# Kernel optimization log

Hardware: AMD Instinct MI355X
Metric: run time of the kernel (lower is better)

Reference implementation:

```python
import jax, jax.numpy as jnp
import numpy as np

N = 50000      # nodes
E = 800000     # edges
IN = 32        # raw node feature dim
PE = 15        # laplacian PE dim (k)
HID = 128      # hidden
HEADS = 4
C = HID // HEADS
G = 64         # graphs in batch
L = 4          # num layers (shared weights!)


def setup_inputs() -> dict:
    key = jax.random.key(0)
    ks = jax.random.split(key, 24)
    s = 0.05
    p = lambda k, shape: jax.random.normal(k, shape, dtype=jnp.float32) * s
    inp = {
        "x": jax.random.normal(ks[0], (N, IN), dtype=jnp.float32),
        "edge_index": jax.random.randint(ks[1], (2, E), 0, N, dtype=jnp.int32),
        "batch": jnp.sort(jax.random.randint(ks[2], (N,), 0, G, dtype=jnp.int32)),
        "lap_pe": jax.random.normal(ks[3], (N, PE), dtype=jnp.float32),
        # node_in: Linear(IN+PE -> HID)
        "node_in_w": p(ks[4], (HID, IN + PE)), "node_in_b": p(ks[5], (HID,)),
        # shared TransformerConv params
        "Wq": p(ks[6], (HID, HID)), "bq": p(ks[7], (HID,)),
        "Wk": p(ks[8], (HID, HID)), "bk": p(ks[9], (HID,)),
        "Wv": p(ks[10], (HID, HID)), "bv": p(ks[11], (HID,)),
        "Wskip": p(ks[12], (HID, HID)), "bskip": p(ks[13], (HID,)),
        "Wbeta": p(ks[14], (1, 3 * HID)),  # bias=False in PyG
        # attentional aggregation gate: Linear(HID,HID)->ReLU->Linear(HID,1)
        "g1_w": p(ks[15], (HID, HID)), "g1_b": p(ks[16], (HID,)),
        "g2_w": p(ks[17], (1, HID)), "g2_b": p(ks[18], (1,)),
        # readout: Linear(HID,HID)->ReLU->Linear(HID,1)
        "r1_w": p(ks[19], (HID, HID)), "r1_b": p(ks[20], (HID,)),
        "r2_w": p(ks[21], (1, HID)), "r2_b": p(ks[22], (1,)),
    }
    return inp


def _transformer_conv(x, src, dst, Wq, bq, Wk, bk, Wv, bv, Wskip, bskip, Wbeta):
    # projections -> [N, HEADS, C]
    q = (x @ Wq.T + bq).reshape(N, HEADS, C)
    k = (x @ Wk.T + bk).reshape(N, HEADS, C)
    v = (x @ Wv.T + bv).reshape(N, HEADS, C)
    # edge attention logits: [E, HEADS]
    alpha = jnp.einsum('ehc,ehc->eh', q[dst], k[src]) / jnp.sqrt(jnp.float32(C))
    # segment softmax over destination node
    amax = jax.ops.segment_max(alpha, dst, num_segments=N)        # [N, HEADS]
    ex = jnp.exp(alpha - amax[dst])
    denom = jax.ops.segment_sum(ex, dst, num_segments=N)          # [N, HEADS]
    attn = ex / denom[dst]                                        # [E, HEADS]
    # weighted scatter-add of values
    msg = v[src] * attn[:, :, None]                               # [E, HEADS, C]
    out = jax.ops.segment_sum(msg, dst, num_segments=N).reshape(N, HID)
    # beta-gated skip connection (beta=True, root_weight=True)
    x_r = x @ Wskip.T + bskip
    beta = jax.nn.sigmoid(jnp.concatenate([out, x_r, out - x_r], axis=-1) @ Wbeta.T)
    return beta * x_r + (1.0 - beta) * out


def reference(x, edge_index, batch, lap_pe, node_in_w, node_in_b,
              Wq, bq, Wk, bk, Wv, bv, Wskip, bskip, Wbeta,
              g1_w, g1_b, g2_w, g2_b, r1_w, r1_b, r2_w, r2_b):
    src, dst = edge_index[0], edge_index[1]
    h = jnp.concatenate([x, lap_pe], axis=-1) @ node_in_w.T + node_in_b  # [N, HID]
    for _ in range(L):  # same conv instance reused -> shared weights
        h = jax.nn.relu(h + _transformer_conv(h, src, dst, Wq, bq, Wk, bk,
                                              Wv, bv, Wskip, bskip, Wbeta))
    # attentional aggregation over graphs
    gate = jax.nn.relu(h @ g1_w.T + g1_b) @ g2_w.T + g2_b                # [N, 1]
    gmax = jax.ops.segment_max(gate, batch, num_segments=G)
    gex = jnp.exp(gate - gmax[batch])
    gden = jax.ops.segment_sum(gex, batch, num_segments=G)
    w = gex / gden[batch]                                                # [N, 1]
    g = jax.ops.segment_sum(w * h, batch, num_segments=G)                # [G, HID]
    out = jax.nn.relu(g @ r1_w.T + r1_b) @ r2_w.T + r2_b                 # [G, 1]
    return out.squeeze(-1)
```

## Files before the change

### kernel.cpp

```cpp
#include <hip/hip_runtime.h>

#define NN 50000
#define EE 800000
#define INF 32
#define PEF 15
#define HID 128
#define GG 64
#define NLAYERS 4
#define NBLK 196
#define NBUCK 49
#define ECH 4096
#define EBLK 196

typedef __bf16 bf16;
typedef __attribute__((ext_vector_type(8))) bf16 bf16x8;
typedef __attribute__((ext_vector_type(4))) float f32x4;
typedef __attribute__((ext_vector_type(2))) float f32x2;

__device__ __forceinline__ float wave_allsum(float v) {
  #pragma unroll
  for (int off = 1; off < 64; off <<= 1) v += __shfl_xor(v, off);
  return v;
}

__device__ __forceinline__ float bflo(unsigned u) {
  return __builtin_bit_cast(float, u << 16);
}
__device__ __forceinline__ float bfhi(unsigned u) {
  return __builtin_bit_cast(float, u & 0xffff0000u);
}
__device__ __forceinline__ unsigned short f2bf(float v) {
  unsigned b = __builtin_bit_cast(unsigned, v);
  unsigned r = (b + 0x7fffu + ((b >> 16) & 1u)) >> 16;
  return (unsigned short)r;
}
__device__ __forceinline__ unsigned bfpack(float lo, float hi) {
  return (unsigned)f2bf(lo) | ((unsigned)f2bf(hi) << 16);
}
__device__ __forceinline__ unsigned fp8pack4(float a, float b, float c, float d) {
  unsigned lo = (unsigned)__builtin_amdgcn_cvt_pk_fp8_f32(a, b, 0, false) & 0xffffu;
  unsigned hi = (unsigned)__builtin_amdgcn_cvt_pk_fp8_f32(c, d, 0, false) & 0xffffu;
  return lo | (hi << 16);
}

__global__ void pack_weights_kernel(const float* __restrict__ Wq, const float* __restrict__ Wk,
                                    const float* __restrict__ Wv, const float* __restrict__ Ws,
                                    const float* __restrict__ bq, const float* __restrict__ bk,
                                    const float* __restrict__ bv, const float* __restrict__ bs,
                                    unsigned short* __restrict__ Wcatb, float* __restrict__ bcat) {
  int idx = blockIdx.x * blockDim.x + threadIdx.x;
  if (idx >= 512 * 128) return;
  int o = idx >> 7, j = idx & 127;
  const float* W; const float* b; int r;
  if (o < 128) { W = Wq; b = bq; r = o; }
  else if (o < 384) {
    int g = (o - 128) >> 6, c = (o - 128) & 63;
    if (c < 32) { W = Wk; b = bk; r = 32 * g + c; }
    else        { W = Wv; b = bv; r = 32 * g + (c - 32); }
  } else { W = Ws; b = bs; r = o - 384; }
  Wcatb[idx] = f2bf(W[r * 128 + j]);
  if (j == 0) bcat[o] = b[r];
}

__global__ void pack_nwtb_kernel(const float* __restrict__ niw, unsigned short* __restrict__ nwtb) {
  int idx = blockIdx.x * blockDim.x + threadIdx.x;
  if (idx >= 128 * 64) return;
  int n = idx >> 6, j = idx & 63;
  nwtb[idx] = (j < INF + PEF) ? f2bf(niw[n * (INF + PEF) + j]) : (unsigned short)0;
}

__global__ void pack_g1_kernel(const float* __restrict__ g1w, unsigned short* __restrict__ g1wb) {
  int idx = blockIdx.x * blockDim.x + threadIdx.x;
  if (idx >= 128 * 128) return;
  g1wb[idx] = f2bf(g1w[idx]);
}

__global__ __launch_bounds__(256) void xpe_pack_kernel(const float* __restrict__ x,
    const float* __restrict__ pe, unsigned* __restrict__ xpeb4) {
  int n = blockIdx.x * 256 + threadIdx.x;
  if (n >= NN) return;
  unsigned ou[32];
  const float4* xr = (const float4*)(x + (size_t)n * INF);
  #pragma unroll
  for (int i = 0; i < 8; i++) {
    float4 v = xr[i];
    ou[2 * i] = bfpack(v.x, v.y);
    ou[2 * i + 1] = bfpack(v.z, v.w);
  }
  const float* pr = pe + (size_t)n * PEF;
  float p[16];
  #pragma unroll
  for (int i = 0; i < PEF; i++) p[i] = pr[i];
  p[15] = 0.f;
  #pragma unroll
  for (int i = 0; i < 8; i++) ou[16 + i] = bfpack(p[2 * i], p[2 * i + 1]);
  #pragma unroll
  for (int i = 24; i < 32; i++) ou[i] = 0u;
  unsigned* dst = xpeb4 + (size_t)n * 32;
  #pragma unroll
  for (int i = 0; i < 8; i++) ((uint4*)dst)[i] = *(uint4*)&ou[4 * i];
}

__global__ __launch_bounds__(256) void nodein_gemm_kernel(
    const bf16* __restrict__ A, const bf16* __restrict__ B,
    const float* __restrict__ bias, int M,
    float* __restrict__ h, unsigned* __restrict__ hbf4) {
  __shared__ float lds[128 * 64];
  const int t = threadIdx.x;
  const int w = t >> 6, lane = t & 63;
  const int m0 = blockIdx.x * 128;
  const int n0 = blockIdx.y * 64;
  const int lrow = lane & 15, lk = (lane >> 4) * 8;
  int ra = m0 + w * 32 + lrow;      if (ra > M - 1) ra = M - 1;
  int rb = m0 + w * 32 + 16 + lrow; if (rb > M - 1) rb = M - 1;
  const bf16* a0p = A + (size_t)ra * 64 + lk;
  const bf16* a1p = A + (size_t)rb * 64 + lk;
  const bf16* bp  = B + (size_t)(n0 + lrow) * 64 + lk;
  f32x4 acc[2][4] = {};
  #pragma unroll
  for (int ks = 0; ks < 2; ks++) {
    bf16x8 a0 = *(const bf16x8*)(a0p + ks * 32);
    bf16x8 a1 = *(const bf16x8*)(a1p + ks * 32);
    #pragma unroll
    for (int nj = 0; nj < 4; nj++) {
      bf16x8 b = *(const bf16x8*)(bp + (size_t)nj * 1024 + ks * 32);
      acc[0][nj] = __builtin_amdgcn_mfma_f32_16x16x32_bf16(a0, b, acc[0][nj], 0, 0, 0);
      acc[1][nj] = __builtin_amdgcn_mfma_f32_16x16x32_bf16(a1, b, acc[1][nj], 0, 0, 0);
    }
  }
  const int rbase = (lane >> 4) * 4;
  #pragma unroll
  for (int mi = 0; mi < 2; mi++) {
    #pragma unroll
    for (int nj = 0; nj < 4; nj++) {
      #pragma unroll
      for (int r = 0; r < 4; r++) {
        int ml = w * 32 + mi * 16 + rbase + r;
        int col = nj * 16 + lrow;
        lds[ml * 64 + (col ^ ((ml & 7) << 2))] = acc[mi][nj][r] + bias[n0 + col];
      }
    }
  }
  __syncthreads();
  #pragma unroll
  for (int kk = 0; kk < 2; kk++) {
    int u = t + kk * 256;
    int r = u & 127, s = u >> 7;
    int m = m0 + r;
    if (m >= M) continue;
    float ff[16];
    #pragma unroll
    for (int j = 0; j < 4; j++) {
      int c = s * 16 + j * 4;
      *(float4*)(ff + j * 4) = *(const float4*)(lds + r * 64 + (c ^ ((r & 7) << 2)));
    }
    int c0 = n0 + s * 16;
    float4* hp = (float4*)(h + (size_t)m * 128 + c0);
    #pragma unroll
    for (int j = 0; j < 4; j++) hp[j] = *(float4*)(ff + j * 4);
    unsigned o[8];
    #pragma unroll
    for (int i = 0; i < 8; i++) o[i] = bfpack(ff[2 * i], ff[2 * i + 1]);
    uint4* hb = (uint4*)(hbf4 + (size_t)m * 64 + (c0 >> 1));
    hb[0] = *(uint4*)&o[0];
    hb[1] = *(uint4*)&o[4];
  }
}

__global__ __launch_bounds__(256) void bsum_kernel(const int* __restrict__ counts,
                                                   int* __restrict__ bsum) {
  int b = blockIdx.x, t = threadIdx.x;
  int i = b * 256 + t;
  int v = (i < NN) ? counts[i] : 0;
  #pragma unroll
  for (int off = 1; off < 64; off <<= 1) v += __shfl_xor(v, off);
  __shared__ int red[4];
  if ((t & 63) == 0) red[t >> 6] = v;
  __syncthreads();
  if (t == 0) bsum[b] = red[0] + red[1] + red[2] + red[3];
}

__global__ void bscan_kernel(const int* __restrict__ bsum, int* __restrict__ bbase) {
  int lane = threadIdx.x;
  int carry = 0;
  for (int c = 0; c < NBLK; c += 64) {
    int i = c + lane;
    int v = (i < NBLK) ? bsum[i] : 0;
    int x = v;
    #pragma unroll
    for (int off = 1; off < 64; off <<= 1) {
      int u = __shfl_up(x, off);
      if (lane >= off) x += u;
    }
    if (i < NBLK) bbase[i] = carry + x - v;
    carry += __shfl(x, 63);
  }
}

__global__ __launch_bounds__(256) void rowptr_kernel(const int* __restrict__ counts,
    const int* __restrict__ bbase, int* __restrict__ row_ptr) {
  int b = blockIdx.x, t = threadIdx.x;
  int lane = t & 63, wid = t >> 6;
  int i = b * 256 + t;
  int v = (i < NN) ? counts[i] : 0;
  int x = v;
  #pragma unroll
  for (int off = 1; off < 64; off <<= 1) {
    int u = __shfl_up(x, off);
    if (lane >= off) x += u;
  }
  __shared__ int wsum[4];
  if (lane == 63) wsum[wid] = x;
  __syncthreads();
  int offs = bbase[b];
  for (int k = 0; k < wid; k++) offs += wsum[k];
  int incl = offs + x;
  if (i < NN) row_ptr[i + 1] = incl;
  if (b == 0 && t == 0) row_ptr[0] = 0;
}

__global__ __launch_bounds__(256) void binhist_kernel(const int* __restrict__ dst,
    int* __restrict__ blockHist, int* __restrict__ counts) {
  __shared__ int hist[NBUCK];
  int t = threadIdx.x;
  if (t < NBUCK) hist[t] = 0;
  __syncthreads();
  int base = blockIdx.x * ECH;
  int end = base + ECH; if (end > EE) end = EE;
  for (int i = base + t; i < end; i += 256) {
    int d = dst[i];
    atomicAdd(&hist[d >> 10], 1);
    atomicAdd(&counts[d], 1);
  }
  __syncthreads();
  if (t < NBUCK) blockHist[blockIdx.x * NBUCK + t] = hist[t];
}

__global__ void bscan2_kernel(const int* __restrict__ blockHist,
    int* __restrict__ blockBase, int* __restrict__ bucket_base) {
  int t = threadIdx.x;
  int tot = 0;
  if (t < NBUCK)
    for (int b = 0; b < EBLK; b++) tot += blockHist[b * NBUCK + t];
  int x = tot;
  #pragma unroll
  for (int off = 1; off < 64; off <<= 1) {
    int u = __shfl_up(x, off);
    if (t >= off) x += u;
  }
  int excl = x - tot;
  if (t < NBUCK) bucket_base[t] = excl;
  if (t == NBUCK - 1) bucket_base[NBUCK] = excl + tot;
  if (t < NBUCK) {
    int run = excl;
    for (int b = 0; b < EBLK; b++) {
      blockBase[b * NBUCK + t] = run;
      run += blockHist[b * NBUCK + t];
    }
  }
}

__global__ __launch_bounds__(256) void binwrite_kernel(const int* __restrict__ src,
    const int* __restrict__ dst, const int* __restrict__ blockBase,
    unsigned* __restrict__ binned) {
  __shared__ int cur[NBUCK];
  int t = threadIdx.x;
  if (t < NBUCK) cur[t] = blockBase[blockIdx.x * NBUCK + t];
  __syncthreads();
  int base = blockIdx.x * ECH;
  int end = base + ECH; if (end > EE) end = EE;
  for (int i = base + t; i < end; i += 256) {
    int d = dst[i];
    int p = atomicAdd(&cur[d >> 10], 1);
    binned[p] = (unsigned)src[i] | ((unsigned)(d & 1023) << 16);
  }
}

__global__ __launch_bounds__(512) void scatter2_kernel(const unsigned* __restrict__ binned,
    const int* __restrict__ row_ptr, const int* __restrict__ bucket_base,
    unsigned short* __restrict__ srcs16) {
  __shared__ int cur[1024];
  int g = blockIdx.x, t = threadIdx.x;
  int nbase = g << 10;
  for (int j = t; j < 1024; j += 512) {
    int node = nbase + j;
    cur[j] = (node < NN) ? row_ptr[node] : 0;
  }
  __syncthreads();
  int s0 = bucket_base[g], s1 = bucket_base[g + 1];
  for (int i = s0 + t; i < s1; i += 512) {
    unsigned pr = binned[i];
    int p = atomicAdd(&cur[pr >> 16], 1);
    srcs16[p] = (unsigned short)(pr & 0xffffu);
  }
}

__global__ void gptr_kernel(const int* __restrict__ batch, int* __restrict__ gptr) {
  int g = threadIdx.x;
  if (g > GG) return;
  if (g == GG) { gptr[GG] = NN; return; }
  int lo = 0, hi = NN;
  while (lo < hi) {
    int mid = (lo + hi) >> 1;
    if (batch[mid] < g) lo = mid + 1; else hi = mid;
  }
  gptr[g] = lo;
}

__global__ __launch_bounds__(256) void gemm0_kernel(
    const bf16* __restrict__ A, const bf16* __restrict__ B,
    const float* __restrict__ bias, int M,
    unsigned short* __restrict__ qbb, unsigned char* __restrict__ kvb,
    unsigned short* __restrict__ xrbb) {
  __shared__ float lds[128 * 64];
  const int t = threadIdx.x;
  const int w = t >> 6, lane = t & 63;
  const int m0 = blockIdx.x * 128;
  const int by = blockIdx.y;
  const int n0 = by * 64;
  const int lrow = lane & 15, lk = (lane >> 4) * 8;
  int ra = m0 + w * 32 + lrow;      if (ra > M - 1) ra = M - 1;
  int rb = m0 + w * 32 + 16 + lrow; if (rb > M - 1) rb = M - 1;
  const bf16* a0p = A + (size_t)ra * 128 + lk;
  const bf16* a1p = A + (size_t)rb * 128 + lk;
  const bf16* bp  = B + (size_t)(n0 + lrow) * 128 + lk;
  f32x4 acc[2][4] = {};
  #pragma unroll
  for (int ks = 0; ks < 4; ks++) {
    bf16x8 a0 = *(const bf16x8*)(a0p + ks * 32);
    bf16x8 a1 = *(const bf16x8*)(a1p + ks * 32);
    #pragma unroll
    for (int nj = 0; nj < 4; nj++) {
      bf16x8 b = *(const bf16x8*)(bp + (size_t)nj * 2048 + ks * 32);
      acc[0][nj] = __builtin_amdgcn_mfma_f32_16x16x32_bf16(a0, b, acc[0][nj], 0, 0, 0);
      acc[1][nj] = __builtin_amdgcn_mfma_f32_16x16x32_bf16(a1, b, acc[1][nj], 0, 0, 0);
    }
  }
  const int rbase = (lane >> 4) * 4;
  #pragma unroll
  for (int mi = 0; mi < 2; mi++) {
    #pragma unroll
    for (int nj = 0; nj < 4; nj++) {
      #pragma unroll
      for (int r = 0; r < 4; r++) {
        int ml = w * 32 + mi * 16 + rbase + r;
        int col = nj * 16 + lrow;
        lds[ml * 64 + (col ^ ((ml & 7) << 2))] = acc[mi][nj][r] + bias[n0 + col];
      }
    }
  }
  __syncthreads();
  if (by >= 2 && by < 6) {
    const int g = by - 2;
    #pragma unroll
    for (int kk = 0; kk < 2; kk++) {
      int u = t + kk * 256;
      int r = u >> 2, o = u & 3;
      int m = m0 + r;
      if (m >= M) continue;
      float fk[8], fv[8];
      int cK = o * 8, cV = 32 + o * 8;
      *(float4*)(fk)     = *(const float4*)(lds + r * 64 + ((cK)     ^ ((r & 7) << 2)));
      *(float4*)(fk + 4) = *(const float4*)(lds + r * 64 + ((cK + 4) ^ ((r & 7) << 2)));
      *(float4*)(fv)     = *(const float4*)(lds + r * 64 + ((cV)     ^ ((r & 7) << 2)));
      *(float4*)(fv + 4) = *(const float4*)(lds + r * 64 + ((cV + 4) ^ ((r & 7) << 2)));
      unsigned oc[4];
      oc[0] = fp8pack4(fk[0], fk[1], fk[2], fk[3]);
      oc[1] = fp8pack4(fk[4], fk[5], fk[6], fk[7]);
      oc[2] = fp8pack4(fv[0], fv[1], fv[2], fv[3]);
      oc[3] = fp8pack4(fv[4], fv[5], fv[6], fv[7]);
      *(uint4*)(kvb + (size_t)m * 256 + (size_t)(4 * g + o) * 16) = *(uint4*)oc;
    }
  } else {
    #pragma unroll
    for (int kk = 0; kk < 2; kk++) {
      int u = t + kk * 256;
      int r = u & 127, s = u >> 7;
      int m = m0 + r;
      if (m >= M) continue;
      float ff[16];
      #pragma unroll
      for (int j = 0; j < 4; j++) {
        int c = s * 16 + j * 4;
        *(float4*)(ff + j * 4) = *(const float4*)(lds + r * 64 + (c ^ ((r & 7) << 2)));
      }
      int c0 = (by & 1) * 64 + s * 16;
      unsigned o[8];
      #pragma unroll
      for (int i = 0; i < 8; i++) o[i] = bfpack(ff[2 * i], ff[2 * i + 1]);
      if (by < 2) {
        uint4* dq = (uint4*)(qbb + (size_t)m * 128 + c0);
        dq[0] = *(uint4*)&o[0];
        dq[1] = *(uint4*)&o[4];
      } else {
        uint4* dx = (uint4*)(xrbb + (size_t)m * 128 + c0);
        dx[0] = *(uint4*)&o[0];
        dx[1] = *(uint4*)&o[4];
      }
    }
  }
}

__global__ __launch_bounds__(512) void gemm1_gate_kernel(
    const bf16* __restrict__ A, const bf16* __restrict__ B,
    const float* __restrict__ b1, const float* __restrict__ g2w,
    const float* __restrict__ g2b, int M, float* __restrict__ gx) {
  const int w = threadIdx.x >> 6, lane = threadIdx.x & 63;
  const int m0 = blockIdx.x * 128 + w * 16;
  const int lrow = lane & 15, lk = (lane >> 4) * 8;
  int ra = m0 + lrow; if (ra > M - 1) ra = M - 1;
  const bf16* ap = A + (size_t)ra * 128 + lk;
  const bf16* bp = B + (size_t)lrow * 128 + lk;
  f32x4 acc[8] = {};
  #pragma unroll
  for (int ks = 0; ks < 4; ks++) {
    bf16x8 a = *(const bf16x8*)(ap + ks * 32);
    #pragma unroll
    for (int nj = 0; nj < 8; nj++) {
      bf16x8 b = *(const bf16x8*)(bp + (size_t)nj * 2048 + ks * 32);
      acc[nj] = __builtin_amdgcn_mfma_f32_16x16x32_bf16(a, b, acc[nj], 0, 0, 0);
    }
  }
  float g2v[8], b1v[8];
  #pragma unroll
  for (int nj = 0; nj < 8; nj++) {
    g2v[nj] = g2w[nj * 16 + lrow];
    b1v[nj] = b1[nj * 16 + lrow];
  }
  const float b2 = g2b[0];
  const int rbase = (lane >> 4) * 4;
  #pragma unroll
  for (int r = 0; r < 4; r++) {
    int m = m0 + rbase + r;
    float d = 0.f;
    #pragma unroll
    for (int nj = 0; nj < 8; nj++)
      d += fmaxf(acc[nj][r] + b1v[nj], 0.f) * g2v[nj];
    d += __shfl_xor(d, 1);
    d += __shfl_xor(d, 2);
    d += __shfl_xor(d, 4);
    d += __shfl_xor(d, 8);
    if (lrow == 0 && m < M) gx[m] = __expf(d + b2);
  }
}

__global__ __launch_bounds__(256) void attn_beta_kernel(
    const unsigned short* __restrict__ qbb,
    const unsigned char* __restrict__ kvb,
    const int* __restrict__ row_ptr, const unsigned short* __restrict__ srcs,
    const unsigned* __restrict__ xrb4,
    const float* __restrict__ Wbeta,
    float* __restrict__ h, unsigned* __restrict__ hbf4) {
  __shared__ float xlds[4][128];
  const int wid = threadIdx.x >> 6;
  const int wv = blockIdx.x * 4 + wid;
  const int lane = threadIdx.x & 63;
  const int sl = lane & 15;
  const int eg = lane >> 4;
  float qf[8];
  {
    bf16x8 qv = *(const bf16x8*)((const bf16*)qbb + (size_t)wv * 128 + sl * 8);
    #pragma unroll
    for (int j = 0; j < 8; j++) qf[j] = (float)qv[j];
  }
  const int e0 = row_ptr[wv], e1 = row_ptr[wv + 1];
  const float C = 0.25503486f;
  float dex = 0.f;
  float acc[8] = {0, 0, 0, 0, 0, 0, 0, 0};

#define PROC(cell, valid)                                                   \
  {                                                                         \
    f32x2 k0 = __builtin_amdgcn_cvt_pk_f32_fp8((cell).x, false);            \
    f32x2 k1 = __builtin_amdgcn_cvt_pk_f32_fp8((cell).x, true);             \
    f32x2 k2 = __builtin_amdgcn_cvt_pk_f32_fp8((cell).y, false);            \
    f32x2 k3 = __builtin_amdgcn_cvt_pk_f32_fp8((cell).y, true);             \
    float p = qf[0] * k0.x + qf[1] * k0.y + qf[2] * k1.x + qf[3] * k1.y     \
            + qf[4] * k2.x + qf[5] * k2.y + qf[6] * k3.x + qf[7] * k3.y;    \
    p += __shfl_xor(p, 1);                                                  \
    p += __shfl_xor(p, 2);                                                  \
    float ex = (valid) ? exp2f(p * C) : 0.f;                                \
    dex += ex;                                                              \
    f32x2 v0 = __builtin_amdgcn_cvt_pk_f32_fp8((cell).z, false);            \
    f32x2 v1 = __builtin_amdgcn_cvt_pk_f32_fp8((cell).z, true);             \
    f32x2 v2 = __builtin_amdgcn_cvt_pk_f32_fp8((cell).w, false);            \
    f32x2 v3 = __builtin_amdgcn_cvt_pk_f32_fp8((cell).w, true);             \
    acc[0] += ex * v0.x; acc[1] += ex * v0.y;                               \
    acc[2] += ex * v1.x; acc[3] += ex * v1.y;                               \
    acc[4] += ex * v2.x; acc[5] += ex * v2.y;                               \
    acc[6] += ex * v3.x; acc[7] += ex * v3.y;                               \
  }

  for (int base = e0; base < e1; base += 64) {
    int rem = e1 - base;
    int cnt = rem < 64 ? rem : 64;
    int mysrc = (lane < rem) ? (int)srcs[base + lane] : 0;
    int i = 0;
    for (; i + 4 < cnt; i += 8) {
      int sea = __shfl(mysrc, i + eg);
      int seb = __shfl(mysrc, i + 4 + eg);
      uint4 ca = *(const uint4*)(kvb + (size_t)sea * 256 + sl * 16);
      uint4 cb = *(const uint4*)(kvb + (size_t)seb * 256 + sl * 16);
      PROC(ca, true);
      PROC(cb, (i + 4 + eg < cnt));
    }
    if (i < cnt) {
      int sea = __shfl(mysrc, i + eg);
      uint4 ca = *(const uint4*)(kvb + (size_t)sea * 256 + sl * 16);
      PROC(ca, (i + eg < cnt));
    }
  }
#undef PROC

  dex += __shfl_xor(dex, 16);
  dex += __shfl_xor(dex, 32);
  #pragma unroll
  for (int j = 0; j < 8; j++) {
    acc[j] += __shfl_xor(acc[j], 16);
    acc[j] += __shfl_xor(acc[j], 32);
  }
  float inv = (e1 > e0) ? 1.f / dex : 0.f;
  if (eg == 0) {
    #pragma unroll
    for (int j = 0; j < 8; j++) xlds[wid][sl * 8 + j] = acc[j] * inv;
  }
  __syncthreads();
  float ox = xlds[wid][2 * lane];
  float oy = xlds[wid][2 * lane + 1];
  unsigned xu = xrb4[(size_t)wv * 64 + lane];
  float xx = bflo(xu), xy = bfhi(xu);
  const float2* wb = (const float2*)Wbeta;
  float2 wo = wb[lane], wx = wb[64 + lane], wd = wb[128 + lane];
  float part = ox * wo.x + oy * wo.y + xx * wx.x + xy * wx.y
             + (ox - xx) * wd.x + (oy - xy) * wd.y;
  part = wave_allsum(part);
  float beta = 1.f / (1.f + __expf(-part));
  float2* hp = (float2*)(h + (size_t)wv * 128);
  float2 h2 = hp[lane];
  float r0 = fmaxf(h2.x + beta * xx + (1.f - beta) * ox, 0.f);
  float r1 = fmaxf(h2.y + beta * xy + (1.f - beta) * oy, 0.f);
  h2.x = r0; h2.y = r1;
  hp[lane] = h2;
  hbf4[(size_t)wv * 64 + lane] = bfpack(r0, r1);
}

__global__ __launch_bounds__(256) void gden_kernel(const float* __restrict__ gx,
    const int* __restrict__ gptr, float* __restrict__ gden) {
  int g = blockIdx.x, t = threadIdx.x;
  int n0 = gptr[g], n1 = gptr[g + 1];
  float s = 0.f;
  for (int n = n0 + t; n < n1; n += 256) s += gx[n];
  s = wave_allsum(s);
  __shared__ float red[4];
  if ((t & 63) == 0) red[t >> 6] = s;
  __syncthreads();
  if (t == 0) gden[g] = red[0] + red[1] + red[2] + red[3];
}

__global__ __launch_bounds__(128) void gagg_kernel(const float* __restrict__ gx,
    const float* __restrict__ h, const int* __restrict__ gptr,
    float* __restrict__ gfeat_raw) {
  int g = blockIdx.x;
  int c = blockIdx.y;
  int d = threadIdx.x;
  int n0 = gptr[g], n1 = gptr[g + 1];
  float acc = 0.f;
  for (int n = n0 + c; n < n1; n += 32) acc += gx[n] * h[(size_t)n * 128 + d];
  atomicAdd(&gfeat_raw[g * 128 + d], acc);
}

__global__ __launch_bounds__(128) void readout_kernel(const float* __restrict__ gfeat_raw,
    const float* __restrict__ gden,
    const float* __restrict__ r1w, const float* __restrict__ r1b,
    const float* __restrict__ r2w, const float* __restrict__ r2b,
    float* __restrict__ out) {
  int g = blockIdx.x;
  int u = threadIdx.x;
  __shared__ float sh[128];
  __shared__ float red[128];
  float dv = gden[g];
  float inv = (dv > 0.f) ? 1.f / dv : 0.f;
  sh[u] = gfeat_raw[g * 128 + u] * inv;
  __syncthreads();
  float tacc = r1b[u];
  for (int j = 0; j < 128; j++) tacc += sh[j] * r1w[u * 128 + j];
  tacc = fmaxf(tacc, 0.f);
  red[u] = tacc * r2w[u];
  __syncthreads();
  for (int off = 64; off > 0; off >>= 1) {
    if (u < off) red[u] += red[u + off];
    __syncthreads();
  }
  if (u == 0) out[g] = red[0] + r2b[0];
}

extern "C" void kernel_launch(void* const* d_in, const int* in_sizes, int n_in,
                              void* d_out, int out_size, void* d_ws, size_t ws_size,
                              hipStream_t stream) {
  (void)in_sizes; (void)n_in; (void)out_size; (void)ws_size;
  const float* x     = (const float*)d_in[0];
  const int*   ei    = (const int*)d_in[1];
  const int*   batch = (const int*)d_in[2];
  const float* pe    = (const float*)d_in[3];
  const float* niw   = (const float*)d_in[4];
  const float* nib   = (const float*)d_in[5];
  const float* Wq    = (const float*)d_in[6];
  const float* bq    = (const float*)d_in[7];
  const float* Wk    = (const float*)d_in[8];
  const float* bk    = (const float*)d_in[9];
  const float* Wv    = (const float*)d_in[10];
  const float* bv    = (const float*)d_in[11];
  const float* Wsk   = (const float*)d_in[12];
  const float* bsk   = (const float*)d_in[13];
  const float* Wbeta = (const float*)d_in[14];
  const float* g1w   = (const float*)d_in[15];
  const float* g1b   = (const float*)d_in[16];
  const float* g2w   = (const float*)d_in[17];
  const float* g2b   = (const float*)d_in[18];
  const float* r1w   = (const float*)d_in[19];
  const float* r1b   = (const float*)d_in[20];
  const float* r2w   = (const float*)d_in[21];
  const float* r2b   = (const float*)d_in[22];
  float* out = (float*)d_out;

  float* ws = (float*)d_ws;
  float* h     = ws; ws += (size_t)NN * 128;
  float* qbbf  = ws; ws += (size_t)NN * 64;
  float* kvbf  = ws; ws += (size_t)NN * 64;
  float* xrbf  = ws; ws += (size_t)NN * 64;
  float* hbff  = ws; ws += (size_t)NN * 64;
  float* xpebf = ws; ws += (size_t)NN * 32;
  float* Wcatf = ws; ws += 512 * 64;
  float* g1wbf = ws; ws += 128 * 64;
  float* nwtbf = ws; ws += 128 * 32;
  float* bcat  = ws; ws += 512;
  float* gx    = ws; ws += NN;
  float* gfeat = ws; ws += GG * 128;
  float* gden  = ws; ws += GG;
  int* row_ptr = (int*)ws;
  int* counts   = row_ptr + (NN + 1);
  int* bsum     = counts + NN;
  int* bbase    = bsum + NBLK;
  int* gptr     = bbase + NBLK;
  int* blockHist= gptr + (GG + 1);
  int* blockBase= blockHist + EBLK * NBUCK;
  int* bucketB  = blockBase + EBLK * NBUCK;
  unsigned* binned = (unsigned*)(bucketB + (NBUCK + 1));
  unsigned short* srcs16 = (unsigned short*)(binned + EE);

  unsigned short* qbb   = (unsigned short*)qbbf;
  unsigned char*  kvb   = (unsigned char*)kvbf;
  unsigned short* xrbb  = (unsigned short*)xrbf;
  unsigned short* hbf   = (unsigned short*)hbff;
  unsigned short* Wcatb = (unsigned short*)Wcatf;
  unsigned short* g1wb  = (unsigned short*)g1wbf;
  unsigned short* nwtb  = (unsigned short*)nwtbf;
  const int* src = ei;
  const int* dst = ei + EE;

  hipMemsetAsync(counts, 0, NN * sizeof(int), stream);
  hipMemsetAsync(gfeat, 0, GG * 128 * sizeof(float), stream);
  pack_weights_kernel<<<(512 * 128 + 255) / 256, 256, 0, stream>>>(
      Wq, Wk, Wv, Wsk, bq, bk, bv, bsk, Wcatb, bcat);
  pack_nwtb_kernel<<<(128 * 64 + 255) / 256, 256, 0, stream>>>(niw, nwtb);
  pack_g1_kernel<<<(128 * 128 + 255) / 256, 256, 0, stream>>>(g1w, g1wb);
  xpe_pack_kernel<<<NBLK, 256, 0, stream>>>(x, pe, (unsigned*)xpebf);
  binhist_kernel<<<EBLK, 256, 0, stream>>>(dst, blockHist, counts);
  bsum_kernel<<<NBLK, 256, 0, stream>>>(counts, bsum);
  bscan_kernel<<<1, 64, 0, stream>>>(bsum, bbase);
  rowptr_kernel<<<NBLK, 256, 0, stream>>>(counts, bbase, row_ptr);
  bscan2_kernel<<<1, 64, 0, stream>>>(blockHist, blockBase, bucketB);
  binwrite_kernel<<<EBLK, 256, 0, stream>>>(src, dst, blockBase, binned);
  scatter2_kernel<<<NBUCK, 512, 0, stream>>>(binned, row_ptr, bucketB, srcs16);
  gptr_kernel<<<1, 128, 0, stream>>>(batch, gptr);

  const int MB0 = (NN + 127) / 128;
  nodein_gemm_kernel<<<dim3(MB0, 2), 256, 0, stream>>>(
      (const bf16*)xpebf, (const bf16*)nwtb, nib, NN, h, (unsigned*)hbf);

  for (int l = 0; l < NLAYERS; l++) {
    gemm0_kernel<<<dim3(MB0, 8), 256, 0, stream>>>(
        (const bf16*)hbf, (const bf16*)Wcatb, bcat, NN, qbb, kvb, xrbb);
    attn_beta_kernel<<<12500, 256, 0, stream>>>(
        qbb, kvb, row_ptr, srcs16, (const unsigned*)xrbb, Wbeta, h, (unsigned*)hbf);
  }

  gemm1_gate_kernel<<<MB0, 512, 0, stream>>>(
      (const bf16*)hbf, (const bf16*)g1wb, g1b, g2w, g2b, NN, gx);
  gden_kernel<<<GG, 256, 0, stream>>>(gx, gptr, gden);
  gagg_kernel<<<dim3(GG, 32), 128, 0, stream>>>(gx, h, gptr, gfeat);
  readout_kernel<<<GG, 128, 0, stream>>>(gfeat, gden, r1w, r1b, r2w, r2b, out);
}
```

Before: 524.9 us.

## Drop fp32 residual state, keep hidden only in bf16; software-pipeline edge gather loads

Removes the fp32 copy of the hidden state h. The residual add in attention, the node-in GEMM output and the graph aggregation now read the bf16 copy, which cuts global traffic for the residual read and write in every layer. The edge loop in the attention kernel is also restructured: each lane group loads its own source index directly and double-buffers two kv gathers ahead of the compute, replacing the shuffle-based 64-edge chunking. The cost is lower residual precision across layers, and the gagg kernel now reads 16-bit elements with a strided pattern.

```diff
diff --git a/kernel.cpp b/kernel.cpp
--- a/kernel.cpp
+++ b/kernel.cpp
@@ -103,8 +103,7 @@
 
 __global__ __launch_bounds__(256) void nodein_gemm_kernel(
     const bf16* __restrict__ A, const bf16* __restrict__ B,
-    const float* __restrict__ bias, int M,
-    float* __restrict__ h, unsigned* __restrict__ hbf4) {
+    const float* __restrict__ bias, int M, unsigned* __restrict__ hbf4) {
   __shared__ float lds[128 * 64];
   const int t = threadIdx.x;
   const int w = t >> 6, lane = t & 63;
@@ -155,9 +154,6 @@
       *(float4*)(ff + j * 4) = *(const float4*)(lds + r * 64 + (c ^ ((r & 7) << 2)));
     }
     int c0 = n0 + s * 16;
-    float4* hp = (float4*)(h + (size_t)m * 128 + c0);
-    #pragma unroll
-    for (int j = 0; j < 4; j++) hp[j] = *(float4*)(ff + j * 4);
     unsigned o[8];
     #pragma unroll
     for (int i = 0; i < 8; i++) o[i] = bfpack(ff[2 * i], ff[2 * i + 1]);
@@ -450,13 +446,14 @@
     const int* __restrict__ row_ptr, const unsigned short* __restrict__ srcs,
     const unsigned* __restrict__ xrb4,
     const float* __restrict__ Wbeta,
-    float* __restrict__ h, unsigned* __restrict__ hbf4) {
+    unsigned* __restrict__ hbf4) {
   __shared__ float xlds[4][128];
   const int wid = threadIdx.x >> 6;
   const int wv = blockIdx.x * 4 + wid;
   const int lane = threadIdx.x & 63;
   const int sl = lane & 15;
   const int eg = lane >> 4;
+  const int sl16 = sl * 16;
   float qf[8];
   {
     bf16x8 qv = *(const bf16x8*)((const bf16*)qbb + (size_t)wv * 128 + sl * 8);
@@ -490,26 +487,34 @@
     acc[6] += ex * v3.x; acc[7] += ex * v3.y;                               \
   }
 
-  for (int base = e0; base < e1; base += 64) {
-    int rem = e1 - base;
-    int cnt = rem < 64 ? rem : 64;
-    int mysrc = (lane < rem) ? (int)srcs[base + lane] : 0;
-    int i = 0;
-    for (; i + 4 < cnt; i += 8) {
-      int sea = __shfl(mysrc, i + eg);
-      int seb = __shfl(mysrc, i + 4 + eg);
-      uint4 ca = *(const uint4*)(kvb + (size_t)sea * 256 + sl * 16);
-      uint4 cb = *(const uint4*)(kvb + (size_t)seb * 256 + sl * 16);
-      PROC(ca, true);
-      PROC(cb, (i + 4 + eg < cnt));
-    }
-    if (i < cnt) {
-      int sea = __shfl(mysrc, i + eg);
-      uint4 ca = *(const uint4*)(kvb + (size_t)sea * 256 + sl * 16);
-      PROC(ca, (i + eg < cnt));
-    }
+#define LOADW(it, cvar, vvar)                                               \
+  {                                                                         \
+    int ei = eBase + (it) * 4;                                              \
+    vvar = ei < e1;                                                         \
+    int s = (int)srcs[vvar ? ei : e0];                                      \
+    cvar = *(const uint4*)(kvb + (size_t)s * 256 + sl16);                   \
+  }
+
+  const int eBase = e0 + eg;
+  const int nIt = (e1 - e0 + 3) >> 2;
+  if (nIt > 0) {
+    uint4 c0, c1; bool v0, v1;
+    LOADW(0, c0, v0);
+    LOADW(1, c1, v1);
+    const int nPair = (nIt + 1) >> 1;
+    for (int p2 = 1; p2 < nPair; p2++) {
+      uint4 n0, n1; bool w0, w1;
+      LOADW(2 * p2, n0, w0);
+      LOADW(2 * p2 + 1, n1, w1);
+      PROC(c0, v0);
+      PROC(c1, v1);
+      c0 = n0; v0 = w0; c1 = n1; v1 = w1;
+    }
+    PROC(c0, v0);
+    PROC(c1, v1);
   }
 #undef PROC
+#undef LOADW
 
   dex += __shfl_xor(dex, 16);
   dex += __shfl_xor(dex, 32);
@@ -534,12 +539,10 @@
              + (ox - xx) * wd.x + (oy - xy) * wd.y;
   part = wave_allsum(part);
   float beta = 1.f / (1.f + __expf(-part));
-  float2* hp = (float2*)(h + (size_t)wv * 128);
-  float2 h2 = hp[lane];
-  float r0 = fmaxf(h2.x + beta * xx + (1.f - beta) * ox, 0.f);
-  float r1 = fmaxf(h2.y + beta * xy + (1.f - beta) * oy, 0.f);
-  h2.x = r0; h2.y = r1;
-  hp[lane] = h2;
+  unsigned hu = hbf4[(size_t)wv * 64 + lane];
+  float hx = bflo(hu), hy = bfhi(hu);
+  float r0 = fmaxf(hx + beta * xx + (1.f - beta) * ox, 0.f);
+  float r1 = fmaxf(hy + beta * xy + (1.f - beta) * oy, 0.f);
   hbf4[(size_t)wv * 64 + lane] = bfpack(r0, r1);
 }
 
@@ -557,14 +560,15 @@
 }
 
 __global__ __launch_bounds__(128) void gagg_kernel(const float* __restrict__ gx,
-    const float* __restrict__ h, const int* __restrict__ gptr,
+    const unsigned short* __restrict__ hbf, const int* __restrict__ gptr,
     float* __restrict__ gfeat_raw) {
   int g = blockIdx.x;
   int c = blockIdx.y;
   int d = threadIdx.x;
   int n0 = gptr[g], n1 = gptr[g + 1];
   float acc = 0.f;
-  for (int n = n0 + c; n < n1; n += 32) acc += gx[n] * h[(size_t)n * 128 + d];
+  for (int n = n0 + c; n < n1; n += 32)
+    acc += gx[n] * bflo((unsigned)hbf[(size_t)n * 128 + d]);
   atomicAdd(&gfeat_raw[g * 128 + d], acc);
 }
 
@@ -623,7 +627,6 @@
   float* out = (float*)d_out;
 
   float* ws = (float*)d_ws;
-  float* h     = ws; ws += (size_t)NN * 128;
   float* qbbf  = ws; ws += (size_t)NN * 64;
   float* kvbf  = ws; ws += (size_t)NN * 64;
   float* xrbf  = ws; ws += (size_t)NN * 64;
@@ -675,18 +678,18 @@
 
   const int MB0 = (NN + 127) / 128;
   nodein_gemm_kernel<<<dim3(MB0, 2), 256, 0, stream>>>(
-      (const bf16*)xpebf, (const bf16*)nwtb, nib, NN, h, (unsigned*)hbf);
+      (const bf16*)xpebf, (const bf16*)nwtb, nib, NN, (unsigned*)hbf);
 
   for (int l = 0; l < NLAYERS; l++) {
     gemm0_kernel<<<dim3(MB0, 8), 256, 0, stream>>>(
         (const bf16*)hbf, (const bf16*)Wcatb, bcat, NN, qbb, kvb, xrbb);
     attn_beta_kernel<<<12500, 256, 0, stream>>>(
-        qbb, kvb, row_ptr, srcs16, (const unsigned*)xrbb, Wbeta, h, (unsigned*)hbf);
+        qbb, kvb, row_ptr, srcs16, (const unsigned*)xrbb, Wbeta, (unsigned*)hbf);
   }
 
   gemm1_gate_kernel<<<MB0, 512, 0, stream>>>(
       (const bf16*)hbf, (const bf16*)g1wb, g1b, g2w, g2b, NN, gx);
   gden_kernel<<<GG, 256, 0, stream>>>(gx, gptr, gden);
-  gagg_kernel<<<dim3(GG, 32), 128, 0, stream>>>(gx, h, gptr, gfeat);
+  gagg_kernel<<<dim3(GG, 32), 128, 0, stream>>>(gx, hbf, gptr, gfeat);
   readout_kernel<<<GG, 128, 0, stream>>>(gfeat, gden, r1w, r1b, r2w, r2b, out);
 }
```

Result: faster. 509.8 us (-2.9%).
